# Performance work log

Measured on AMD Instinct MI355X. Metric: run time of the kernel, lower is better.

## Reference

```python
import jax, jax.numpy as jnp
import numpy as np

N, E = 50000, 800000
D_IN, D_HID, D_OUT = 128, 256, 128


def setup_inputs() -> dict:
    key = jax.random.key(0)
    k = jax.random.split(key, 7)
    x = jax.random.normal(k[0], (N, D_IN), dtype=jnp.float32)
    edge_src = jax.random.randint(k[1], (E,), 0, N, dtype=jnp.int32)
    edge_dst = jax.random.randint(k[2], (E,), 0, N, dtype=jnp.int32)
    s1 = 1.0 / np.sqrt(2 * D_IN)
    s2 = 1.0 / np.sqrt(2 * D_HID)
    W1 = jax.random.uniform(k[3], (2 * D_IN, D_HID), jnp.float32, -s1, s1)
    b1 = jax.random.uniform(k[4], (D_HID,), jnp.float32, -s1, s1)
    W2 = jax.random.uniform(k[5], (2 * D_HID, D_OUT), jnp.float32, -s2, s2)
    b2 = jax.random.uniform(k[6], (D_OUT,), jnp.float32, -s2, s2)
    return {"x": x, "edge_src": edge_src, "edge_dst": edge_dst,
            "W1": W1, "b1": b1, "W2": W2, "b2": b2}


def _sage_layer(h, edge_src, edge_dst, W, b, inv_deg):
    # mean-pool neighbor features: gather [E, D] then segment-sum to [N, D]
    msgs = h[edge_src]
    agg = jax.ops.segment_sum(msgs, edge_dst, num_segments=h.shape[0]) * inv_deg
    y = jnp.concatenate([h, agg], axis=1)  # [N, 2D]
    return y @ W + b


def reference(x, edge_src, edge_dst, W1, b1, W2, b2):
    n = x.shape[0]
    deg = jax.ops.segment_sum(jnp.ones_like(edge_dst, dtype=x.dtype), edge_dst,
                              num_segments=n)
    inv_deg = (1.0 / jnp.maximum(deg, 1.0))[:, None]  # isolated nodes -> zeros
    h = _sage_layer(x, edge_src, edge_dst, W1, b1, inv_deg)
    h = jax.nn.relu(h)
    # dropout is identity in eval mode
    h = _sage_layer(h, edge_src, edge_dst, W2, b2, inv_deg)
    return jax.nn.log_softmax(h, axis=1)
```

## Files before the change

kernel.cpp:

```cpp
#include <hip/hip_runtime.h>
#include <cstdint>
#include <cstddef>

typedef __attribute__((ext_vector_type(8))) short bf16x8;
typedef __attribute__((ext_vector_type(4))) float f32x4;
typedef __attribute__((ext_vector_type(2))) float f32x2;

__device__ inline short bf16_rne(float f) {
  unsigned u = __builtin_bit_cast(unsigned, f);
  u += 0x7fff + ((u >> 16) & 1);
  return (short)(u >> 16);
}

__device__ inline float bf16lo(unsigned v) { return __builtin_bit_cast(float, v << 16); }
__device__ inline float bf16hi(unsigned v) { return __builtin_bit_cast(float, v & 0xffff0000u); }

__device__ inline unsigned pack2(float a, float b) {
  return ((unsigned)(unsigned short)bf16_rne(a)) | (((unsigned)(unsigned short)bf16_rne(b)) << 16);
}

__device__ inline void async_copy16(const void* g, void* l) {
  __builtin_amdgcn_global_load_lds((const __attribute__((address_space(1))) void*)g,
                                   (__attribute__((address_space(3))) void*)l, 16, 0, 0);
}


__global__ __launch_bounds__(256) void prep_kernel(const float* __restrict__ W1,
                                                   const float* __restrict__ W2,
                                                   const float* __restrict__ b2,
                                                   const float* __restrict__ x,
                                                   short* __restrict__ B1p,
                                                   short* __restrict__ B2p,
                                                   float* __restrict__ bias2,
                                                   unsigned* __restrict__ A1u,
                                                   unsigned* __restrict__ xf8, int nquads,
                                                   int* __restrict__ counters, int NB) {
  int b = blockIdx.x;
  int tid = threadIdx.x;
  int nqb = (nquads + 255) >> 8;
  if (b < 512) {
    int mode = b >> 8;
    int idx = (b & 255) * 256 + tid;
    int j = idx & 7;
    int L = (idx >> 3) & 63;
    int nt = (idx >> 9) & 15;
    int kb = idx >> 13;
    int k = kb * 32 + (L >> 4) * 8 + j;
    int n = nt * 16 + (L & 15);
    if (mode == 0) {
      B1p[idx] = bf16_rne(W1[(size_t)k * 256 + n]);
    } else {
      float v = (n < 128) ? W2[(size_t)k * 128 + n] : W2[(size_t)(256 + k) * 128 + (n - 128)];
      B2p[idx] = bf16_rne(v);
    }
  } else if (b == 512) {
    bias2[tid] = (tid < 128) ? b2[tid] : 0.0f;
  } else if (b < 513 + nqb) {
    int idx = (b - 513) * 256 + tid;
    if (idx < nquads) {
      int n = idx >> 5, q = idx & 31;
      float4 v = ((const float4*)x)[idx];
      ((uint2*)A1u)[(size_t)n * 64 + q] = make_uint2(pack2(v.x, v.y), pack2(v.z, v.w));
      int pk = __builtin_amdgcn_cvt_pk_fp8_f32(v.x, v.y, 0, false);
      pk = __builtin_amdgcn_cvt_pk_fp8_f32(v.z, v.w, pk, true);
      xf8[(size_t)n * 32 + q] = (unsigned)pk;
    }
  } else {
    for (int t = tid; t < NB; t += 256) counters[t] = 0;
  }
}

__global__ __launch_bounds__(256) void bucket_scatter(const int* __restrict__ src,
                                                      const int* __restrict__ dst, int E, int EPB,
                                                      int* __restrict__ counters, int NB,
                                                      int SLACK, unsigned* __restrict__ bedge) {
  __shared__ int h[512];
  __shared__ int base[512];
  int tid = threadIdx.x;
  for (int t = tid; t < NB; t += 256) h[t] = 0;
  __syncthreads();
  int start = blockIdx.x * EPB, end = min(E, start + EPB);
  for (int i = start + tid; i < end; i += 256) atomicAdd(&h[((unsigned)dst[i]) >> 7], 1);
  __syncthreads();
  for (int t = tid; t < NB; t += 256) {
    int c = h[t];
    base[t] = (c > 0) ? atomicAdd(&counters[t], c) : 0;
    h[t] = 0;
  }
  __syncthreads();
  for (int i = start + tid; i < end; i += 256) {
    unsigned d = (unsigned)dst[i];
    unsigned bk = d >> 7;
    int p = base[bk] + atomicAdd(&h[bk], 1);
    bedge[(size_t)bk * SLACK + p] = ((d & 127u) << 24) | (unsigned)src[i];
  }
}

__global__ __launch_bounds__(256) void build_csr(const unsigned* __restrict__ bedge,
                                                 const int* __restrict__ counters,
                                                 int NB, int SLACK, int N,
                                                 int* __restrict__ offsets,
                                                 int* __restrict__ oend,
                                                 float* __restrict__ inv_deg,
                                                 int* __restrict__ ssrc) {
  __shared__ int buf[128];
  int b = blockIdx.x, tid = threadIdx.x;
  int cntE = counters[b];
  int rb = b * SLACK;
  if (tid < 128) buf[tid] = 0;
  __syncthreads();
  for (int i = tid; i < cntE; i += 256) atomicAdd(&buf[bedge[(size_t)rb + i] >> 24], 1);
  __syncthreads();
  int cnt = (tid < 128) ? buf[tid] : 0;
  #pragma unroll
  for (int off = 1; off < 128; off <<= 1) {
    int t = (tid >= off && tid < 128) ? buf[tid - off] : 0;
    __syncthreads();
    if (tid < 128) buf[tid] += t;
    __syncthreads();
  }
  if (tid < 128) {
    int excl_l = buf[tid] - cnt;
    int node = (b << 7) + tid;
    if (node < N) {
      offsets[node] = rb + excl_l;
      oend[node]    = rb + excl_l + cnt;
      inv_deg[node] = 1.0f / fmaxf((float)cnt, 1.0f);
    }
    buf[tid] = rb + excl_l;
  }
  __syncthreads();
  for (int i = tid; i < cntE; i += 256) {
    unsigned e2 = bedge[(size_t)rb + i];
    int p = atomicAdd(&buf[e2 >> 24], 1);
    ssrc[p] = (int)(e2 & 0xFFFFFFu);
  }
}

#define CVT8(U, A0, A1, A2, A3, A4, A5, A6, A7)                                        \
  {                                                                                    \
    f32x2 p_, q_;                                                                      \
    p_ = __builtin_amdgcn_cvt_pk_f32_fp8((U).x, false);                                \
    q_ = __builtin_amdgcn_cvt_pk_f32_fp8((U).x, true);                                 \
    A0 += p_[0]; A1 += p_[1]; A2 += q_[0]; A3 += q_[1];                                \
    p_ = __builtin_amdgcn_cvt_pk_f32_fp8((U).y, false);                                \
    q_ = __builtin_amdgcn_cvt_pk_f32_fp8((U).y, true);                                 \
    A4 += p_[0]; A5 += p_[1]; A6 += q_[0]; A7 += q_[1];                                \
  }

__global__ __launch_bounds__(256) void agg1_kernel(const uint2* __restrict__ X8,
                                                   const int* __restrict__ offsets,
                                                   const int* __restrict__ oend,
                                                   const int* __restrict__ ssrc,
                                                   const float* __restrict__ inv_deg,
                                                   uint4* __restrict__ A1q, int N) {
  int node = blockIdx.x * 4 + (threadIdx.x >> 6);
  if (node >= N) return;
  int lane = threadIdx.x & 63;
  int g = lane >> 4;
  int l = lane & 15;
  int s = offsets[node], e = oend[node];
  float a0=0.f,a1=0.f,a2=0.f,a3=0.f,a4=0.f,a5=0.f,a6=0.f,a7=0.f;
  int i = s;
  for (; i + 16 <= e; i += 16) {
    int sA = ssrc[i + g], sB = ssrc[i + 4 + g];
    int sC = ssrc[i + 8 + g], sD = ssrc[i + 12 + g];
    uint2 u = X8[((size_t)(unsigned)sA << 4) + l];
    uint2 v = X8[((size_t)(unsigned)sB << 4) + l];
    uint2 w = X8[((size_t)(unsigned)sC << 4) + l];
    uint2 z = X8[((size_t)(unsigned)sD << 4) + l];
    CVT8(u, a0,a1,a2,a3,a4,a5,a6,a7);
    CVT8(v, a0,a1,a2,a3,a4,a5,a6,a7);
    CVT8(w, a0,a1,a2,a3,a4,a5,a6,a7);
    CVT8(z, a0,a1,a2,a3,a4,a5,a6,a7);
  }
  for (; i < e; i += 4) {
    if (g < e - i) {
      uint2 u = X8[((size_t)(unsigned)ssrc[i + g] << 4) + l];
      CVT8(u, a0,a1,a2,a3,a4,a5,a6,a7);
    }
  }
  a0 += __shfl_xor(a0,16,64); a0 += __shfl_xor(a0,32,64);
  a1 += __shfl_xor(a1,16,64); a1 += __shfl_xor(a1,32,64);
  a2 += __shfl_xor(a2,16,64); a2 += __shfl_xor(a2,32,64);
  a3 += __shfl_xor(a3,16,64); a3 += __shfl_xor(a3,32,64);
  a4 += __shfl_xor(a4,16,64); a4 += __shfl_xor(a4,32,64);
  a5 += __shfl_xor(a5,16,64); a5 += __shfl_xor(a5,32,64);
  a6 += __shfl_xor(a6,16,64); a6 += __shfl_xor(a6,32,64);
  a7 += __shfl_xor(a7,16,64); a7 += __shfl_xor(a7,32,64);
  if (g == 0) {
    float id = inv_deg[node];
    A1q[((size_t)node << 5) + 16 + l] =
        make_uint4(pack2(a0 * id, a1 * id), pack2(a2 * id, a3 * id),
                   pack2(a4 * id, a5 * id), pack2(a6 * id, a7 * id));
  }
}

__global__ __launch_bounds__(256) void gemm_mfma(const short* __restrict__ A,
                                                 const short* __restrict__ Bp,
                                                 const float* __restrict__ bias,
                                                 void* __restrict__ out0,
                                                 void* __restrict__ out1,
                                                 int M_pad, int mode) {
  __shared__ __align__(16) short As[4096];
  __shared__ __align__(16) short Bs[4096];
  int tid = threadIdx.x;
  int w = tid >> 6;
  int lane = tid & 63;
  int wr = w >> 1;
  int wc = w & 1;
  int bm = blockIdx.x * 128;
  int bn = blockIdx.y * 128;

  f32x4 acc[4][4];
  #pragma unroll
  for (int i = 0; i < 4; ++i)
    #pragma unroll
    for (int j = 0; j < 4; ++j) acc[i][j] = (f32x4)(0.0f);

  for (int kb = 0; kb < 8; ++kb) {
    #pragma unroll
    for (int q = 0; q < 2; ++q) {
      int f = q * 4 + w;
      int row = bm + f * 16 + (lane & 15);
      const short* g = A + (size_t)row * 256 + kb * 32 + (lane >> 4) * 8;
      async_copy16(g, &As[f * 512]);
    }
    #pragma unroll
    for (int q = 0; q < 2; ++q) {
      int f = q * 4 + w;
      const short* g = Bp + ((size_t)(kb * 16 + (bn >> 4) + f) * 64 + lane) * 8;
      async_copy16(g, &Bs[f * 512]);
    }
    __syncthreads();

    bf16x8 af[4], bfr[4];
    #pragma unroll
    for (int i = 0; i < 4; ++i)
      af[i] = *(const bf16x8*)&As[(wr * 4 + i) * 512 + lane * 8];
    #pragma unroll
    for (int j = 0; j < 4; ++j)
      bfr[j] = *(const bf16x8*)&Bs[(wc * 4 + j) * 512 + lane * 8];

    #pragma unroll
    for (int i = 0; i < 4; ++i)
      #pragma unroll
      for (int j = 0; j < 4; ++j)
        acc[i][j] = __builtin_amdgcn_mfma_f32_16x16x32_bf16(af[i], bfr[j], acc[i][j], 0, 0, 0);
    __syncthreads();
  }

  int crow0 = (lane >> 4) * 4;
  int ccol = lane & 15;
  #pragma unroll
  for (int i = 0; i < 4; ++i) {
    #pragma unroll
    for (int j = 0; j < 4; ++j) {
      int col_loc = wc * 64 + j * 16 + ccol;
      int col = bn + col_loc;
      #pragma unroll
      for (int r = 0; r < 4; ++r) {
        int row = bm + wr * 64 + i * 16 + crow0 + r;
        float v = acc[i][j][r] + bias[col];
        if (mode == 0) {
          v = fmaxf(v, 0.0f);
          ((short*)out0)[(size_t)row * 256 + col] = bf16_rne(v);
        } else if (blockIdx.y == 0) {
          ((short*)out0)[(size_t)row * 128 + col_loc] = bf16_rne(v);
        } else {
          int pk = __builtin_amdgcn_cvt_pk_fp8_f32(v, v, 0, false);
          ((unsigned char*)out1)[(size_t)row * 128 + col_loc] = (unsigned char)(pk & 0xff);
        }
      }
    }
  }
}

__global__ __launch_bounds__(256) void final_kernel(const uint4* __restrict__ utopq,
                                                    const uint2* __restrict__ T2,
                                                    const int* __restrict__ offsets,
                                                    const int* __restrict__ oend,
                                                    const int* __restrict__ ssrc,
                                                    const float* __restrict__ inv_deg,
                                                    float4* __restrict__ out4, int N) {
  int node = blockIdx.x * 4 + (threadIdx.x >> 6);
  if (node >= N) return;
  int lane = threadIdx.x & 63;
  int g = lane >> 4;
  int l = lane & 15;
  int s = offsets[node], e = oend[node];
  float a0=0.f,a1=0.f,a2=0.f,a3=0.f,a4=0.f,a5=0.f,a6=0.f,a7=0.f;
  int i = s;
  for (; i + 16 <= e; i += 16) {
    int sA = ssrc[i + g], sB = ssrc[i + 4 + g];
    int sC = ssrc[i + 8 + g], sD = ssrc[i + 12 + g];
    uint2 u = T2[((size_t)(unsigned)sA << 4) + l];
    uint2 v = T2[((size_t)(unsigned)sB << 4) + l];
    uint2 w = T2[((size_t)(unsigned)sC << 4) + l];
    uint2 z = T2[((size_t)(unsigned)sD << 4) + l];
    CVT8(u, a0,a1,a2,a3,a4,a5,a6,a7);
    CVT8(v, a0,a1,a2,a3,a4,a5,a6,a7);
    CVT8(w, a0,a1,a2,a3,a4,a5,a6,a7);
    CVT8(z, a0,a1,a2,a3,a4,a5,a6,a7);
  }
  for (; i < e; i += 4) {
    if (g < e - i) {
      uint2 u = T2[((size_t)(unsigned)ssrc[i + g] << 4) + l];
      CVT8(u, a0,a1,a2,a3,a4,a5,a6,a7);
    }
  }
  a0 += __shfl_xor(a0,16,64); a0 += __shfl_xor(a0,32,64);
  a1 += __shfl_xor(a1,16,64); a1 += __shfl_xor(a1,32,64);
  a2 += __shfl_xor(a2,16,64); a2 += __shfl_xor(a2,32,64);
  a3 += __shfl_xor(a3,16,64); a3 += __shfl_xor(a3,32,64);
  a4 += __shfl_xor(a4,16,64); a4 += __shfl_xor(a4,32,64);
  a5 += __shfl_xor(a5,16,64); a5 += __shfl_xor(a5,32,64);
  a6 += __shfl_xor(a6,16,64); a6 += __shfl_xor(a6,32,64);
  a7 += __shfl_xor(a7,16,64); a7 += __shfl_xor(a7,32,64);
  if (g == 0) {
    float id = inv_deg[node];
    uint4 U = utopq[((size_t)node << 4) + l];
    float v0 = bf16lo(U.x) + a0 * id;
    float v1 = bf16hi(U.x) + a1 * id;
    float v2 = bf16lo(U.y) + a2 * id;
    float v3 = bf16hi(U.y) + a3 * id;
    float v4 = bf16lo(U.z) + a4 * id;
    float v5 = bf16hi(U.z) + a5 * id;
    float v6 = bf16lo(U.w) + a6 * id;
    float v7 = bf16hi(U.w) + a7 * id;
    float m = fmaxf(fmaxf(fmaxf(v0, v1), fmaxf(v2, v3)), fmaxf(fmaxf(v4, v5), fmaxf(v6, v7)));
    #pragma unroll
    for (int off = 1; off < 16; off <<= 1) m = fmaxf(m, __shfl_xor(m, off, 16));
    float su = expf(v0 - m) + expf(v1 - m) + expf(v2 - m) + expf(v3 - m) +
               expf(v4 - m) + expf(v5 - m) + expf(v6 - m) + expf(v7 - m);
    #pragma unroll
    for (int off = 1; off < 16; off <<= 1) su += __shfl_xor(su, off, 16);
    float ls = m + logf(su);
    out4[((size_t)node << 5) + l * 2]     = make_float4(v0 - ls, v1 - ls, v2 - ls, v3 - ls);
    out4[((size_t)node << 5) + l * 2 + 1] = make_float4(v4 - ls, v5 - ls, v6 - ls, v7 - ls);
  }
}

extern "C" void kernel_launch(void* const* d_in, const int* in_sizes, int n_in,
                              void* d_out, int out_size, void* d_ws, size_t ws_size,
                              hipStream_t stream) {
  const float* x        = (const float*)d_in[0];
  const int*   edge_src = (const int*)d_in[1];
  const int*   edge_dst = (const int*)d_in[2];
  const float* W1       = (const float*)d_in[3];
  const float* b1       = (const float*)d_in[4];
  const float* W2       = (const float*)d_in[5];
  const float* b2       = (const float*)d_in[6];
  float* out = (float*)d_out;

  const int D_IN = 128;
  const int N = in_sizes[0] / D_IN;
  const int E = in_sizes[1];
  const int M_pad = ((N + 127) / 128) * 128;

  const int SB = 512;
  const int EPB = (E + SB - 1) / SB;
  const int NB = (N + 127) >> 7;
  const int SLACK = 3072;

  char* ws = (char*)d_ws;
  size_t p = 0;
  auto take = [&](size_t bytes) -> size_t {
    size_t r = p;
    p += (bytes + 255) & ~(size_t)255;
    return r;
  };
  size_t cnt_off   = take((size_t)NB * 4);
  size_t bedge_off = take((size_t)NB * SLACK * 4);
  size_t offs_off  = take((size_t)N * 4);
  size_t oend_off  = take((size_t)N * 4);
  size_t inv_off   = take((size_t)N * 4);
  size_t ssrc_off  = take((size_t)NB * SLACK * 4);
  size_t A1_off    = take((size_t)M_pad * 256 * 2);
  size_t xf8_off   = take((size_t)M_pad * 128);
  size_t h_off     = take((size_t)M_pad * 256 * 2);
  size_t B1p_off   = take((size_t)256 * 256 * 2);
  size_t B2p_off   = take((size_t)256 * 256 * 2);
  size_t bias2_off = take((size_t)256 * 4);
  size_t utop_off  = take((size_t)M_pad * 128 * 2);
  size_t t2_off    = take((size_t)M_pad * 128);
  (void)ws_size;

  int*   counters = (int*)(ws + cnt_off);
  unsigned* bedge = (unsigned*)(ws + bedge_off);
  int*   offsets  = (int*)(ws + offs_off);
  int*   oendp    = (int*)(ws + oend_off);
  float* inv_deg  = (float*)(ws + inv_off);
  int*   ssrc     = (int*)(ws + ssrc_off);
  unsigned* A1u   = (unsigned*)(ws + A1_off);
  unsigned* xf8   = (unsigned*)(ws + xf8_off);
  short* h        = (short*)(ws + h_off);
  short* B1p      = (short*)(ws + B1p_off);
  short* B2p      = (short*)(ws + B2p_off);
  float* bias2    = (float*)(ws + bias2_off);
  short* utop     = (short*)(ws + utop_off);
  unsigned char* t2f8 = (unsigned char*)(ws + t2_off);

  {
    int nquads = N * 32;
    int grid = 513 + (nquads + 255) / 256 + 1;
    prep_kernel<<<grid, 256, 0, stream>>>(W1, W2, b2, x, B1p, B2p, bias2, A1u, xf8, nquads,
                                          counters, NB);
  }
  bucket_scatter<<<SB, 256, 0, stream>>>(edge_src, edge_dst, E, EPB, counters, NB, SLACK, bedge);
  build_csr<<<NB, 256, 0, stream>>>(bedge, counters, NB, SLACK, N, offsets, oendp, inv_deg, ssrc);

  agg1_kernel<<<(N + 3) / 4, 256, 0, stream>>>((const uint2*)xf8, offsets, oendp, ssrc, inv_deg,
                                               (uint4*)A1u, N);
  {
    dim3 grid(M_pad / 128, 2);
    gemm_mfma<<<grid, 256, 0, stream>>>((const short*)A1u, B1p, b1, h, nullptr, M_pad, 0);
  }
  {
    dim3 grid(M_pad / 128, 2);
    gemm_mfma<<<grid, 256, 0, stream>>>(h, B2p, bias2, utop, t2f8, M_pad, 1);
  }
  final_kernel<<<(N + 3) / 4, 256, 0, stream>>>((const uint4*)utop, (const uint2*)t2f8,
                                                offsets, oendp, ssrc, inv_deg, (float4*)out, N);
}
```

Measured before the change: 228.8 us.

## Rewrite GEMM as persistent kernel with register-resident weights and 16-row strips

The LDS-tiled 128x128 MFMA GEMM is replaced by a persistent kernel that keeps the full 256-deep K slice of B for its 64 columns in registers (32 bf16x8 per lane). It loops over 16-row strips of A loaded straight from global memory, with no shared memory or barriers. The grid is fixed at 1024 blocks and each block covers all 256 output columns. This aims to remove LDS staging and sync overhead and to reuse weights across many row strips, at the cost of heavy register pressure and A being read by all four waves without sharing through LDS.

```diff
diff --git a/kernel.cpp b/kernel.cpp
--- a/kernel.cpp
+++ b/kernel.cpp
@@ -17,11 +17,6 @@
 
 __device__ inline unsigned pack2(float a, float b) {
   return ((unsigned)(unsigned short)bf16_rne(a)) | (((unsigned)(unsigned short)bf16_rne(b)) << 16);
-}
-
-__device__ inline void async_copy16(const void* g, void* l) {
-  __builtin_amdgcn_global_load_lds((const __attribute__((address_space(1))) void*)g,
-                                   (__attribute__((address_space(3))) void*)l, 16, 0, 0);
 }
 
 
@@ -196,80 +191,62 @@
   }
 }
 
-__global__ __launch_bounds__(256) void gemm_mfma(const short* __restrict__ A,
-                                                 const short* __restrict__ Bp,
-                                                 const float* __restrict__ bias,
-                                                 void* __restrict__ out0,
-                                                 void* __restrict__ out1,
-                                                 int M_pad, int mode) {
-  __shared__ __align__(16) short As[4096];
-  __shared__ __align__(16) short Bs[4096];
+__global__ __launch_bounds__(256, 2) void gemm_mfma(const short* __restrict__ A,
+                                                    const short* __restrict__ Bp,
+                                                    const float* __restrict__ bias,
+                                                    void* __restrict__ out0,
+                                                    void* __restrict__ out1,
+                                                    int S, int mode) {
   int tid = threadIdx.x;
   int w = tid >> 6;
   int lane = tid & 63;
-  int wr = w >> 1;
-  int wc = w & 1;
-  int bm = blockIdx.x * 128;
-  int bn = blockIdx.y * 128;
-
-  f32x4 acc[4][4];
+
+  bf16x8 breg[8][4];
   #pragma unroll
-  for (int i = 0; i < 4; ++i)
-    #pragma unroll
-    for (int j = 0; j < 4; ++j) acc[i][j] = (f32x4)(0.0f);
-
-  for (int kb = 0; kb < 8; ++kb) {
-    #pragma unroll
-    for (int q = 0; q < 2; ++q) {
-      int f = q * 4 + w;
-      int row = bm + f * 16 + (lane & 15);
-      const short* g = A + (size_t)row * 256 + kb * 32 + (lane >> 4) * 8;
-      async_copy16(g, &As[f * 512]);
-    }
-    #pragma unroll
-    for (int q = 0; q < 2; ++q) {
-      int f = q * 4 + w;
-      const short* g = Bp + ((size_t)(kb * 16 + (bn >> 4) + f) * 64 + lane) * 8;
-      async_copy16(g, &Bs[f * 512]);
-    }
-    __syncthreads();
-
-    bf16x8 af[4], bfr[4];
-    #pragma unroll
-    for (int i = 0; i < 4; ++i)
-      af[i] = *(const bf16x8*)&As[(wr * 4 + i) * 512 + lane * 8];
+  for (int kb = 0; kb < 8; ++kb)
     #pragma unroll
     for (int j = 0; j < 4; ++j)
-      bfr[j] = *(const bf16x8*)&Bs[(wc * 4 + j) * 512 + lane * 8];
-
-    #pragma unroll
-    for (int i = 0; i < 4; ++i)
+      breg[kb][j] = *(const bf16x8*)(Bp + ((size_t)((kb * 16 + w * 4 + j) * 64 + lane)) * 8);
+
+  float bj[4];
+  #pragma unroll
+  for (int j = 0; j < 4; ++j) bj[j] = bias[w * 64 + j * 16 + (lane & 15)];
+
+  int rowInFrag = lane & 15;
+  int kseg = (lane >> 4) * 8;
+
+  for (int s = blockIdx.x; s < S; s += gridDim.x) {
+    int row0 = s * 16;
+    const short* Arow = A + (size_t)(row0 + rowInFrag) * 256 + kseg;
+    bf16x8 afr[8];
+    #pragma unroll
+    for (int kb = 0; kb < 8; ++kb) afr[kb] = *(const bf16x8*)(Arow + kb * 32);
+
+    f32x4 acc[4];
+    #pragma unroll
+    for (int j = 0; j < 4; ++j) acc[j] = (f32x4)(0.0f);
+    #pragma unroll
+    for (int kb = 0; kb < 8; ++kb)
       #pragma unroll
       for (int j = 0; j < 4; ++j)
-        acc[i][j] = __builtin_amdgcn_mfma_f32_16x16x32_bf16(af[i], bfr[j], acc[i][j], 0, 0, 0);
-    __syncthreads();
-  }
-
-  int crow0 = (lane >> 4) * 4;
-  int ccol = lane & 15;
-  #pragma unroll
-  for (int i = 0; i < 4; ++i) {
+        acc[j] = __builtin_amdgcn_mfma_f32_16x16x32_bf16(afr[kb], breg[kb][j], acc[j], 0, 0, 0);
+
+    int crow0 = row0 + (lane >> 4) * 4;
+    int ccol = lane & 15;
     #pragma unroll
     for (int j = 0; j < 4; ++j) {
-      int col_loc = wc * 64 + j * 16 + ccol;
-      int col = bn + col_loc;
+      int col = w * 64 + j * 16 + ccol;
       #pragma unroll
       for (int r = 0; r < 4; ++r) {
-        int row = bm + wr * 64 + i * 16 + crow0 + r;
-        float v = acc[i][j][r] + bias[col];
+        float v = acc[j][r] + bj[j];
+        int row = crow0 + r;
         if (mode == 0) {
-          v = fmaxf(v, 0.0f);
-          ((short*)out0)[(size_t)row * 256 + col] = bf16_rne(v);
-        } else if (blockIdx.y == 0) {
-          ((short*)out0)[(size_t)row * 128 + col_loc] = bf16_rne(v);
+          ((short*)out0)[(size_t)row * 256 + col] = bf16_rne(fmaxf(v, 0.0f));
+        } else if (w < 2) {
+          ((short*)out0)[(size_t)row * 128 + col] = bf16_rne(v);
         } else {
           int pk = __builtin_amdgcn_cvt_pk_fp8_f32(v, v, 0, false);
-          ((unsigned char*)out1)[(size_t)row * 128 + col_loc] = (unsigned char)(pk & 0xff);
+          ((unsigned char*)out1)[(size_t)row * 128 + (col - 128)] = (unsigned char)(pk & 0xff);
         }
       }
     }
@@ -413,12 +390,9 @@
   agg1_kernel<<<(N + 3) / 4, 256, 0, stream>>>((const uint2*)xf8, offsets, oendp, ssrc, inv_deg,
                                                (uint4*)A1u, N);
   {
-    dim3 grid(M_pad / 128, 2);
-    gemm_mfma<<<grid, 256, 0, stream>>>((const short*)A1u, B1p, b1, h, nullptr, M_pad, 0);
-  }
-  {
-    dim3 grid(M_pad / 128, 2);
-    gemm_mfma<<<grid, 256, 0, stream>>>(h, B2p, bias2, utop, t2f8, M_pad, 1);
+    int S = M_pad / 16;
+    gemm_mfma<<<1024, 256, 0, stream>>>((const short*)A1u, B1p, b1, h, nullptr, S, 0);
+    gemm_mfma<<<1024, 256, 0, stream>>>(h, B2p, bias2, utop, t2f8, S, 1);
   }
   final_kernel<<<(N + 3) / 4, 256, 0, stream>>>((const uint4*)utop, (const uint2*)t2f8,
                                                 offsets, oendp, ssrc, inv_deg, (float4*)out, N);
```

After: 221.4 us, median of 2. 3.2% less time.
